# Optimization experiments

Hardware: AMD Instinct MI355X
Metric: run time of the kernel (lower is better)

The kernel has to match this reference:

```python
import jax, jax.numpy as jnp
import numpy as np

GROUP_SIZE = 128
IN_FEATURES = 8192
OUT_FEATURES = 28672
TOKENS = 32


def _dequantize(qweight, qzeros, scales):
    """ExLlama q4 dequant.
    qweight: (K//8, N) int32, 8 int4 values per word packed along k.
    qzeros:  (G, N//8) int32, 8 int4 zeros per word packed along n.
    scales:  (G, N) fp16.  g = k // GROUP_SIZE; w = s * (q - (z + 1)).
    """
    shifts = jnp.arange(8, dtype=jnp.int32) * 4
    K = qweight.shape[0] * 8
    N = qweight.shape[1]
    G = qzeros.shape[0]
    # unpack weights along k: (K//8, 8, N) -> (K, N)
    q = (qweight[:, None, :] >> shifts[None, :, None]) & 15
    q = q.reshape(K, N)
    # unpack zeros along n: (G, N//8, 8) -> (G, N)
    z = (qzeros[:, :, None] >> shifts[None, None, :]) & 15
    z = z.reshape(G, N)
    # group-wise dequant: reshape k into (G, GROUP_SIZE)
    qg = q.reshape(G, GROUP_SIZE, N).astype(jnp.float16)
    zf = (z + 1).astype(jnp.float16)[:, None, :]          # ExLlama stores zero-1
    w = (qg - zf) * scales[:, None, :]                    # (G, GS, N) fp16
    return w.reshape(K, N)


def setup_inputs() -> dict:
    key = jax.random.key(0)
    k1, k2, k3, k4, k5 = jax.random.split(key, 5)
    x = jax.random.normal(k1, (TOKENS, IN_FEATURES), dtype=jnp.float16)
    qweight = jax.random.randint(k2, (IN_FEATURES // 8, OUT_FEATURES),
                                 minval=-(2**31), maxval=2**31 - 1, dtype=jnp.int32)
    qzeros = jax.random.randint(k3, (IN_FEATURES // GROUP_SIZE, OUT_FEATURES // 8),
                                minval=-(2**31), maxval=2**31 - 1, dtype=jnp.int32)
    scales = (jax.random.uniform(k4, (IN_FEATURES // GROUP_SIZE, OUT_FEATURES),
                                 dtype=jnp.float32) * 0.01 + 0.001).astype(jnp.float16)
    bias = jax.random.normal(k5, (OUT_FEATURES,), dtype=jnp.float16)
    return {"x": x, "qweight": qweight, "qzeros": qzeros,
            "scales": scales, "bias": bias}


def reference(x, qweight, qzeros, scales, bias):
    w = _dequantize(qweight, qzeros, scales)              # (K, N) fp16
    out = jnp.matmul(x.astype(jnp.float16), w)            # (T, N)
    return out + bias
```

## Files before the change

### kernel.cpp

```cpp
#include <hip/hip_runtime.h>

#define T_TOK   32
#define KDIM    8192
#define NDIM    28672
#define NGRP    64
#define NZWORDS 3584
#define NSEG    16
#define SEGK    (KDIM / NSEG)
#define GPS     (NGRP / NSEG)
#define XROW    (SEGK + 8)

typedef _Float16 half8  __attribute__((ext_vector_type(8)));
typedef _Float16 half2v __attribute__((ext_vector_type(2)));
typedef float    f32x4  __attribute__((ext_vector_type(4)));
typedef unsigned uint4v __attribute__((ext_vector_type(4)));

__global__ __launch_bounds__(256)
void exllama_gemm_deep(const int*   __restrict__ qweight,
                       const int*   __restrict__ qzeros,
                       const float* __restrict__ scales,
                       const float* __restrict__ x,
                       const float* __restrict__ bias,
                       float*       __restrict__ out)
{
    __shared__ alignas(16) _Float16 xs[T_TOK * XROW];

    const int tid  = threadIdx.x;
    const int lane = tid & 63;
    const int wav  = tid >> 6;
    const int quad = lane >> 4;
    const int l16  = lane & 15;
    const int seg  = blockIdx.y;
    const int n0   = blockIdx.x * 256 + wav * 64;

    int nc[4];
    #pragma unroll
    for (int j = 0; j < 4; ++j) nc[j] = n0 + j * 16 + l16;

    const int g0 = seg * GPS;

    unsigned qw[GPS][16];
    half2v   sp[GPS][4], cp[GPS][4];
    #pragma unroll
    for (int g = 0; g < GPS; ++g) {
        const size_t rb = (size_t)((g0 + g) * 16 + quad) * NDIM;
        #pragma unroll
        for (int c = 0; c < 4; ++c)
            #pragma unroll
            for (int j = 0; j < 4; ++j)
                qw[g][c * 4 + j] = (unsigned)qweight[rb + (size_t)(c * 4) * NDIM + nc[j]];
    }
    #pragma unroll
    for (int g = 0; g < GPS; ++g) {
        #pragma unroll
        for (int j = 0; j < 4; ++j) {
            float s  = scales[(size_t)(g0 + g) * NDIM + nc[j]];
            int   zw = qzeros[(size_t)(g0 + g) * NZWORDS + (nc[j] >> 3)];
            int   z  = (zw >> ((nc[j] & 7) * 4)) & 15;
            _Float16 sh = (_Float16)s;
            _Float16 ch = (_Float16)(float)(-(1025 + z));
            sp[g][j] = (half2v){sh, sh};
            cp[g][j] = (half2v){ch, ch};
        }
    }

    {
        const int kseg0 = seg * SEGK;
        #pragma unroll
        for (int it = 0; it < (T_TOK * SEGK) / (256 * 8); ++it) {
            const int e  = it * 2048 + tid * 8;
            const int t  = e >> 9;
            const int kl = e & (SEGK - 1);
            const float* xp = x + (size_t)t * KDIM + kseg0 + kl;
            f32x4 lo = *(const f32x4*)xp;
            f32x4 hi = *(const f32x4*)(xp + 4);
            uint4v u;
            #pragma unroll
            for (int j = 0; j < 4; ++j)
                u[j] = __builtin_bit_cast(unsigned,
                          __builtin_amdgcn_cvt_pkrtz(lo[j], hi[j]));
            *(uint4v*)(xs + t * XROW + kl) = u;
        }
    }
    __syncthreads();

    f32x4 acc[4][2];
    #pragma unroll
    for (int j = 0; j < 4; ++j)
        #pragma unroll
        for (int m = 0; m < 2; ++m)
            acc[j][m] = (f32x4){0.f, 0.f, 0.f, 0.f};

    #pragma unroll
    for (int g = 0; g < GPS; ++g) {
        #pragma unroll
        for (int c = 0; c < 4; ++c) {
            const int kloc = g * 128 + c * 32 + quad * 8;
            half8 a0 = *(const half8*)(xs + l16 * XROW + kloc);
            half8 a1 = *(const half8*)(xs + (l16 + 16) * XROW + kloc);
            #pragma unroll
            for (int j = 0; j < 4; ++j) {
                const unsigned w = qw[g][c * 4 + j];
                uint4v bu;
                #pragma unroll
                for (int i = 0; i < 4; ++i) {
                    unsigned t = ((w >> (4 * i)) & 0x000F000Fu) | 0x64006400u;
                    half2v th = __builtin_bit_cast(half2v, t);
                    half2v r  = (th + cp[g][j]) * sp[g][j];
                    bu[i] = __builtin_bit_cast(unsigned, r);
                }
                half8 bf = __builtin_bit_cast(half8, bu);
                acc[j][0] = __builtin_amdgcn_mfma_f32_16x16x32_f16(a0, bf, acc[j][0], 0, 0, 0);
                acc[j][1] = __builtin_amdgcn_mfma_f32_16x16x32_f16(a1, bf, acc[j][1], 0, 0, 0);
            }
        }
    }

    #pragma unroll
    for (int j = 0; j < 4; ++j) {
        const int n  = n0 + j * 16 + l16;
        const float bb = bias[n] * (1.0f / NSEG);
        #pragma unroll
        for (int m = 0; m < 2; ++m)
            #pragma unroll
            for (int r = 0; r < 4; ++r) {
                const int t = m * 16 + quad * 4 + r;
                unsafeAtomicAdd(out + (size_t)t * NDIM + n, acc[j][m][r] + bb);
            }
    }
}

extern "C" void kernel_launch(void* const* d_in, const int* in_sizes, int n_in,
                              void* d_out, int out_size, void* d_ws, size_t ws_size,
                              hipStream_t stream)
{
    const float* x  = (const float*)d_in[0];
    const int* qweight = (const int*)d_in[1];
    const int* qzeros  = (const int*)d_in[2];
    const float* sc = (const float*)d_in[3];
    const float* bs = (const float*)d_in[4];
    float* out      = (float*)d_out;
    (void)d_ws; (void)ws_size;

    exllama_gemm_deep<<<dim3(NDIM / 256, NSEG), 256, 0, stream>>>(
        qweight, qzeros, sc, x, bs, out);
}
```

Measured before the change: 208.1 us.

## Replace split-K atomic accumulation with workspace partials and a separate reduce kernel

Result: faster. 202.3 us (-2.8%).

```diff
diff --git a/kernel.cpp b/kernel.cpp
--- a/kernel.cpp
+++ b/kernel.cpp
@@ -15,12 +15,14 @@
 typedef float    f32x4  __attribute__((ext_vector_type(4)));
 typedef unsigned uint4v __attribute__((ext_vector_type(4)));
 
+template<bool ATOMIC>
 __global__ __launch_bounds__(256)
 void exllama_gemm_deep(const int*   __restrict__ qweight,
                        const int*   __restrict__ qzeros,
                        const float* __restrict__ scales,
                        const float* __restrict__ x,
                        const float* __restrict__ bias,
+                       float*       __restrict__ ws,
                        float*       __restrict__ out)
 {
     __shared__ alignas(16) _Float16 xs[T_TOK * XROW];
@@ -116,18 +118,48 @@
         }
     }
 
+    if (ATOMIC) {
+        #pragma unroll
+        for (int j = 0; j < 4; ++j) {
+            const int n  = n0 + j * 16 + l16;
+            const float bb = bias[n] * (1.0f / NSEG);
+            #pragma unroll
+            for (int m = 0; m < 2; ++m)
+                #pragma unroll
+                for (int r = 0; r < 4; ++r) {
+                    const int t = m * 16 + quad * 4 + r;
+                    unsafeAtomicAdd(out + (size_t)t * NDIM + n, acc[j][m][r] + bb);
+                }
+        }
+    } else {
+        float* wsp = ws + (size_t)seg * (T_TOK * NDIM);
+        #pragma unroll
+        for (int j = 0; j < 4; ++j) {
+            const int n = n0 + j * 16 + l16;
+            #pragma unroll
+            for (int m = 0; m < 2; ++m)
+                #pragma unroll
+                for (int r = 0; r < 4; ++r) {
+                    const int t = m * 16 + quad * 4 + r;
+                    wsp[(size_t)t * NDIM + n] = acc[j][m][r];
+                }
+        }
+    }
+}
+
+__global__ __launch_bounds__(256)
+void reduce_bias(const float* __restrict__ ws,
+                 const float* __restrict__ bias,
+                 float*       __restrict__ out)
+{
+    const int e = (blockIdx.x * 256 + threadIdx.x) * 4;
+    const int n = e % NDIM;
+    f32x4 sum = (f32x4){0.f, 0.f, 0.f, 0.f};
     #pragma unroll
-    for (int j = 0; j < 4; ++j) {
-        const int n  = n0 + j * 16 + l16;
-        const float bb = bias[n] * (1.0f / NSEG);
-        #pragma unroll
-        for (int m = 0; m < 2; ++m)
-            #pragma unroll
-            for (int r = 0; r < 4; ++r) {
-                const int t = m * 16 + quad * 4 + r;
-                unsafeAtomicAdd(out + (size_t)t * NDIM + n, acc[j][m][r] + bb);
-            }
-    }
+    for (int s = 0; s < NSEG; ++s)
+        sum += *(const f32x4*)(ws + (size_t)s * (T_TOK * NDIM) + e);
+    f32x4 bb = *(const f32x4*)(bias + n);
+    *(f32x4*)(out + e) = sum + bb;
 }
 
 extern "C" void kernel_launch(void* const* d_in, const int* in_sizes, int n_in,
@@ -140,8 +172,15 @@
     const float* sc = (const float*)d_in[3];
     const float* bs = (const float*)d_in[4];
     float* out      = (float*)d_out;
-    (void)d_ws; (void)ws_size;
 
-    exllama_gemm_deep<<<dim3(NDIM / 256, NSEG), 256, 0, stream>>>(
-        qweight, qzeros, sc, x, bs, out);
+    const size_t need = (size_t)NSEG * T_TOK * NDIM * sizeof(float);
+    if (ws_size >= need) {
+        exllama_gemm_deep<false><<<dim3(NDIM / 256, NSEG), 256, 0, stream>>>(
+            qweight, qzeros, sc, x, bs, (float*)d_ws, out);
+        reduce_bias<<<(T_TOK * NDIM) / (256 * 4), 256, 0, stream>>>(
+            (const float*)d_ws, bs, out);
+    } else {
+        exllama_gemm_deep<true><<<dim3(NDIM / 256, NSEG), 256, 0, stream>>>(
+            qweight, qzeros, sc, x, bs, nullptr, out);
+    }
 }
```
